# Performance work log

Hardware: AMD Instinct MI355X
Metric: run time of the kernel (lower is better)

The kernel has to match this reference:

```python
import jax, jax.numpy as jnp
import numpy as np

# ---- module constants (from init_kwargs / zounds.SR22050) ----
SEQ = 64
N_SAMPLES = 16384
N_EVENTS = 16
N_HARM = 32
NOISE_WS = 512
NOISE_STEP = 256
NYQ = 11025.0  # SR22050 nyquist
MIN_F0 = 20.0 / NYQ
MAX_F0 = 800.0 / NYQ
F0_DIFF = MAX_F0 - MIN_F0
HARM_FACTOR = jnp.arange(2, 2 + N_HARM, dtype=jnp.float32)  # [2..33]


def lin_interp(x, size):
    """torch F.interpolate(mode='linear', align_corners=False) along last dim."""
    L = x.shape[-1]
    pos = (jnp.arange(size, dtype=x.dtype) + 0.5) * (L / size) - 0.5
    pos = jnp.clip(pos, 0.0, L - 1)
    i0 = jnp.floor(pos).astype(jnp.int32)
    i1 = jnp.minimum(i0 + 1, L - 1)
    w = (pos - i0).astype(x.dtype)
    return x[..., i0] * (1.0 - w) + x[..., i1] * w


def band_filtered_noise(noise_frames, mean, std):
    """Per-frame Gaussian band-pass of white noise in the STFT domain, overlap-add.
    noise_frames: (b,e,F,ws); mean/std: (b,e,F) in normalized freq [0,1]."""
    ws = noise_frames.shape[-1]
    n = jnp.arange(ws, dtype=noise_frames.dtype)
    win = 0.5 - 0.5 * jnp.cos(2.0 * jnp.pi * n / ws)  # Hann
    spec = jnp.fft.rfft(noise_frames * win, axis=-1)  # (b,e,F,ws//2+1)
    freqs = jnp.linspace(0.0, 1.0, ws // 2 + 1)
    filt = jnp.exp(-0.5 * ((freqs[None, None, None, :] - mean[..., None]) / std[..., None]) ** 2)
    frames = jnp.fft.irfft(spec * filt, n=ws, axis=-1)  # (b,e,F,ws)
    # overlap-add with hop NOISE_STEP (ws == 2*step -> two half-chunks per frame)
    b, e, Fn, _ = frames.shape
    chunks = frames.reshape(b, e, Fn, 2, NOISE_STEP)
    a = chunks[..., 0, :].reshape(b, e, Fn * NOISE_STEP)
    c = chunks[..., 1, :].reshape(b, e, Fn * NOISE_STEP)
    out = jnp.zeros((b, e, (Fn + 1) * NOISE_STEP), dtype=frames.dtype)
    out = out.at[..., : Fn * NOISE_STEP].add(a)
    out = out.at[..., NOISE_STEP:].add(c)
    return out[..., :N_SAMPLES]


def setup_inputs() -> dict:
    key = jax.random.key(0)
    ks = jax.random.split(key, 8)
    B = 8
    return {
        "f0": jax.random.uniform(ks[0], (B, N_EVENTS, SEQ), jnp.float32),
        "overall_env": jax.random.uniform(ks[1], (B, N_EVENTS, SEQ), jnp.float32),
        "osc_env": jax.random.uniform(ks[2], (B, N_EVENTS, SEQ), jnp.float32),
        "noise_env": jax.random.uniform(ks[3], (B, N_EVENTS, SEQ), jnp.float32),
        "harm_env": jax.random.uniform(ks[4], (B, N_EVENTS, N_HARM, SEQ), jnp.float32),
        "noise_std": jax.random.uniform(ks[5], (B, N_EVENTS, SEQ), jnp.float32),
        "f0_baselines": jax.random.uniform(ks[6], (B, N_EVENTS, 1), jnp.float32),
        "noise_frames": jax.random.normal(ks[7], (B, N_EVENTS, SEQ, NOISE_WS), jnp.float32),
    }


def reference(f0, overall_env, osc_env, noise_env, harm_env, noise_std, f0_baselines, noise_frames):
    # f0_baselines branch (ERB-scaled deviation around baseline)
    f0 = jnp.clip(f0, -0.5, 0.5)
    scaled_erb = (0.108 * (f0_baselines * NYQ) + 24.7) / NYQ
    f0 = f0_baselines + f0 * scaled_erb

    orig_f0 = f0 = jnp.clip(f0, 0.0, 1.0)
    overall_env = jnp.clip(overall_env, 0.0, 1.0)
    osc_env = jnp.clip(osc_env, 0.0, 1.0)
    harm_env = jnp.clip(harm_env, 0.0, 1.0)
    noise_std = jnp.clip(noise_std, 1e-12, 1.0)

    f0n = MIN_F0 + f0 * F0_DIFF                                   # (b,e,S)
    harm_f = f0n[:, :, None, :] * HARM_FACTOR[None, None, :, None]  # (b,e,H,S)
    harm_env = osc_env[:, :, None, :] * harm_env                  # (b,e,H,S)

    fund = lin_interp(f0n, N_SAMPLES)           # (b,e,N)
    harm_f_i = lin_interp(harm_f, N_SAMPLES)    # (b,e,H,N)
    osc_env_i = lin_interp(osc_env, N_SAMPLES)  # (b,e,N)
    harm_env_i = lin_interp(harm_env, N_SAMPLES)

    fundamental = jnp.sin(jnp.cumsum(fund * jnp.pi, axis=-1)) * osc_env_i
    harmonics = (jnp.sin(jnp.cumsum(harm_f_i * jnp.pi, axis=-1)) * harm_env_i).sum(axis=-2)
    osc = fundamental + harmonics

    noise_mean = MIN_F0 + orig_f0 * F0_DIFF
    nstd = noise_std * F0_DIFF
    noise = band_filtered_noise(noise_frames, noise_mean, nstd)

    osc_mix = lin_interp(overall_env, N_SAMPLES)
    noise_mix = lin_interp(1.0 - overall_env, N_SAMPLES)
    return osc * osc_mix + noise * noise_mix
```

## Files before the change

### kernel.cpp

```cpp
#include <hip/hip_runtime.h>
#include <math.h>

#define SEQ 64
#define NSAMP 16384
#define NHARM 32
#define NWS 512
#define NSTEP 256
#define BE 128
#define NFRAMES 8192

typedef _Float16 half8 __attribute__((ext_vector_type(8)));
typedef float f32x4 __attribute__((ext_vector_type(4)));

__device__ __forceinline__ float sin_rev(float x) {
  float r; asm("v_sin_f32 %0, %1" : "=v"(r) : "v"(x)); return r;
}
__device__ __forceinline__ float cos_rev(float x) {
  float r; asm("v_cos_f32 %0, %1" : "=v"(r) : "v"(x)); return r;
}
__device__ __forceinline__ float clip01(float v) { return fminf(fmaxf(v, 0.0f), 1.0f); }

__device__ __forceinline__ float f0_to_norm(float f0v, float bl) {
  const float NYQ = 11025.0f;
  const float MIN_F0 = 20.0f / 11025.0f;
  const float F0_DIFF = 780.0f / 11025.0f;
  float v = fminf(fmaxf(f0v, -0.5f), 0.5f);
  float erb = (0.108f * (bl * NYQ) + 24.7f) / NYQ;
  float fv = clip01(bl + v * erb);
  return MIN_F0 + fv * F0_DIFF;
}

__global__ __launch_bounds__(256) void prep_k(_Float16* __restrict__ W1) {
  const int m = blockIdx.x, k = m & 127;
  const int tid = threadIdx.x;
  const bool isSin = m >= 128;
  for (int n = tid; n < 512; n += 256) {
    int a = (k * n) & 511;
    float ph = (float)a * (1.0f / 512.0f);
    W1[m * 512 + n] = (_Float16)(isSin ? sin_rev(ph) : cos_rev(ph));
  }
}

__global__ __launch_bounds__(256) void gemmf_k(const float* __restrict__ Af,
                                               const _Float16* __restrict__ B,
                                               _Float16* __restrict__ Cout,
                                               _Float16* __restrict__ W2,
                                               const float* __restrict__ f0,
                                               const float* __restrict__ nstd,
                                               const float* __restrict__ f0b) {
  const int tid = threadIdx.x;

  if (blockIdx.x < 256) {
    const int k = tid & 127;
    const bool isSin = tid >= 128;
#pragma unroll
    for (int rr = 0; rr < 2; ++rr) {
      const int n = blockIdx.x * 2 + rr;
      int a = (k * n) & 511;
      float ph = (float)a * (1.0f / 512.0f);
      W2[n * 256 + tid] = (_Float16)(isSin ? sin_rev(ph) : cos_rev(ph));
    }
    return;
  }

  const int p = blockIdx.x - 256;
  const int x = p & 7, j = p >> 3;
  const int mstripe = ((j >> 2) << 3) + x;
  const int bn0 = (j & 3) * 64;
  const int m0 = mstripe * 64;

  const int Kt = 512;
  const int wave = tid >> 6, lane = tid & 63;
  const int r = lane & 15, q = lane >> 4;
  __shared__ __align__(16) _Float16 Ash[2][64 * 64];
  __shared__ __align__(16) _Float16 Bsh[2][64 * 64];
  __shared__ __align__(16) float whann[512];

  const int nT = Kt >> 6;
  const int srow0 = tid >> 3, srow1 = (256 + tid) >> 3;
  const int skg = tid & 7;

  half8 ra[2], rb[2];
  f32x4 acc[4] = {};

  whann[tid] = 0.5f - 0.5f * cos_rev((float)tid * (1.0f / 512.0f));
  whann[tid + 256] = 0.5f - 0.5f * cos_rev((float)(tid + 256) * (1.0f / 512.0f));
  __syncthreads();

  auto load_a = [&](int kk) {
    const float* s0 = Af + (size_t)(m0 + srow0) * Kt + kk + skg * 8;
    const float* s1 = Af + (size_t)(m0 + srow1) * Kt + kk + skg * 8;
    float4 a0 = ((const float4*)s0)[0], a1 = ((const float4*)s0)[1];
    float4 b0 = ((const float4*)s1)[0], b1 = ((const float4*)s1)[1];
    float4 w0 = *(const float4*)(&whann[kk + skg * 8]);
    float4 w1 = *(const float4*)(&whann[kk + skg * 8 + 4]);
    ra[0][0] = (_Float16)(a0.x * w0.x); ra[0][1] = (_Float16)(a0.y * w0.y);
    ra[0][2] = (_Float16)(a0.z * w0.z); ra[0][3] = (_Float16)(a0.w * w0.w);
    ra[0][4] = (_Float16)(a1.x * w1.x); ra[0][5] = (_Float16)(a1.y * w1.y);
    ra[0][6] = (_Float16)(a1.z * w1.z); ra[0][7] = (_Float16)(a1.w * w1.w);
    ra[1][0] = (_Float16)(b0.x * w0.x); ra[1][1] = (_Float16)(b0.y * w0.y);
    ra[1][2] = (_Float16)(b0.z * w0.z); ra[1][3] = (_Float16)(b0.w * w0.w);
    ra[1][4] = (_Float16)(b1.x * w1.x); ra[1][5] = (_Float16)(b1.y * w1.y);
    ra[1][6] = (_Float16)(b1.z * w1.z); ra[1][7] = (_Float16)(b1.w * w1.w);
    rb[0] = *(const half8*)(B + (size_t)(bn0 + srow0) * Kt + kk + skg * 8);
    rb[1] = *(const half8*)(B + (size_t)(bn0 + srow1) * Kt + kk + skg * 8);
  };
  auto store_lds = [&](int b) {
    *(half8*)(&Ash[b][srow0 * 64 + ((skg ^ (srow0 & 7)) << 3)]) = ra[0];
    *(half8*)(&Ash[b][srow1 * 64 + ((skg ^ (srow1 & 7)) << 3)]) = ra[1];
    *(half8*)(&Bsh[b][srow0 * 64 + ((skg ^ (srow0 & 7)) << 3)]) = rb[0];
    *(half8*)(&Bsh[b][srow1 * 64 + ((skg ^ (srow1 & 7)) << 3)]) = rb[1];
  };

  load_a(0);
  store_lds(0);

  for (int t = 0;;) {
    if (t + 1 < nT) load_a((t + 1) << 6);
    __syncthreads();
    const int b = t & 1;
#pragma unroll
    for (int ks = 0; ks < 2; ++ks) {
      const int swz = ((ks * 4 + q) ^ (r & 7)) << 3;
      half8 af = *(const half8*)(&Ash[b][(wave * 16 + r) * 64 + swz]);
      half8 bf0 = *(const half8*)(&Bsh[b][(0 * 16 + r) * 64 + swz]);
      half8 bf1 = *(const half8*)(&Bsh[b][(1 * 16 + r) * 64 + swz]);
      half8 bf2 = *(const half8*)(&Bsh[b][(2 * 16 + r) * 64 + swz]);
      half8 bf3 = *(const half8*)(&Bsh[b][(3 * 16 + r) * 64 + swz]);
      acc[0] = __builtin_amdgcn_mfma_f32_16x16x32_f16(af, bf0, acc[0], 0, 0, 0);
      acc[1] = __builtin_amdgcn_mfma_f32_16x16x32_f16(af, bf1, acc[1], 0, 0, 0);
      acc[2] = __builtin_amdgcn_mfma_f32_16x16x32_f16(af, bf2, acc[2], 0, 0, 0);
      acc[3] = __builtin_amdgcn_mfma_f32_16x16x32_f16(af, bf3, acc[3], 0, 0, 0);
    }
    if (t + 1 >= nT) break;
    __syncthreads();
    store_lds((t + 1) & 1);
    ++t;
  }

  const float F0_DIFF = 780.0f / 11025.0f;
#pragma unroll
  for (int reg = 0; reg < 4; ++reg) {
    const int row = m0 + wave * 16 + q * 4 + reg;
    const float mu = f0_to_norm(f0[row], f0b[row >> 6]);
    const float sd = fminf(fmaxf(nstd[row], 1e-12f), 1.0f) * F0_DIFF;
    const float inv_sd = 1.0f / sd;
    const float a = inv_sd * (1.0f / 256.0f);
    const float bmu = mu * inv_sd;
#pragma unroll
    for (int ni = 0; ni < 4; ++ni) {
      const int col = bn0 + ni * 16 + r;
      const int k = col & 127;
      float z = fmaf((float)k, a, -bmu);
      float cf = (k == 0) ? (1.0f / 512.0f) : (2.0f / 512.0f);
      float s = cf * exp2f(z * z * -0.72134752044f);
      Cout[(size_t)row * 256 + col] = (_Float16)(acc[ni][reg] * s);
    }
  }
}

__global__ __launch_bounds__(256) void invfin_k(const _Float16* __restrict__ AB,
                                                const _Float16* __restrict__ W2,
                                                const float* __restrict__ f0,
                                                const float* __restrict__ f0b,
                                                const float* __restrict__ oenv_g,
                                                const float* __restrict__ oscenv_g,
                                                const float* __restrict__ henv_g,
                                                float* __restrict__ out) {
  const int p = blockIdx.x;
  const int x = p & 7, j = p >> 3;
  const int be = ((j >> 2) << 3) + x;
  const int n0 = (j & 3) * 64;
  const int m0 = be * 64;
  const int tid = threadIdx.x;
  const int wave = tid >> 6, lane = tid & 63;
  const int r = lane & 15, q = lane >> 4;

  __shared__ __align__(16) _Float16 Ash[65 * 64];
  __shared__ __align__(16) _Float16 B1sh[64 * 64];
  __shared__ __align__(16) _Float16 B2sh[64 * 64];
  __shared__ __align__(16) float4 qe4[8 * SEQ];
  __shared__ float oenv[SEQ], oscE[SEQ];
  __shared__ float Fs[SEQ], Ds[SEQ], Gs[SEQ];

  if (tid < SEQ) {
    oenv[tid] = clip01(oenv_g[be * SEQ + tid]);
    oscE[tid] = clip01(oscenv_g[be * SEQ + tid]);
    Fs[tid] = f0_to_norm(f0[be * SEQ + tid], f0b[be]);
  }
  __syncthreads();

  if (tid < SEQ) {
    const int s = tid;
    float fcur = Fs[s];
    float fnxt = (s < 63) ? Fs[s + 1] : Fs[63];
    Ds[s] = fnxt - fcur;
    double term = 128.0 * ((double)fcur + (double)fnxt);
    double sc = term;
#pragma unroll
    for (int off = 1; off < 64; off <<= 1) {
      double u = __shfl_up(sc, off, 64);
      if (s >= off) sc += u;
    }
    double C = 128.0 * (double)Fs[0] + (sc - term);
    Gs[s] = (float)(C - 2.0 * floor(C * 0.5));
  }

  for (int idx = tid; idx < 8 * SEQ; idx += 256) {
    int hq = idx >> 6, s = idx & 63;
    const float* hb = henv_g + (size_t)be * (NHARM * SEQ) + (4 * hq) * SEQ + s;
    float e = oscE[s];
    qe4[idx] = make_float4(e * clip01(hb[0]), e * clip01(hb[64]),
                           e * clip01(hb[128]), e * clip01(hb[192]));
  }

  auto stage_AB = [&](int kk) {
#pragma unroll
    for (int it = 0; it < 3; ++it) {
      int g = it * 256 + tid;
      if (g < 520) {
        int row = g >> 3, kg = g & 7;
        half8 v = {0, 0, 0, 0, 0, 0, 0, 0};
        if (row > 0)
          v = *(const half8*)(AB + (size_t)(m0 - 1 + row) * 256 + kk + kg * 8);
        *(half8*)(&Ash[row * 64 + ((kg ^ (row & 7)) << 3)]) = v;
      }
    }
#pragma unroll
    for (int it = 0; it < 4; ++it) {
      int g = it * 256 + tid;
      int row = (g >> 3) & 63, kg = g & 7;
      bool second = g >= 512;
      int wrow = n0 + row + (second ? 256 : 0);
      half8 v = *(const half8*)(W2 + (size_t)wrow * 256 + kk + kg * 8);
      _Float16* dst = second ? B2sh : B1sh;
      *(half8*)(&dst[row * 64 + ((kg ^ (row & 7)) << 3)]) = v;
    }
  };

  f32x4 acc[4] = {};
  stage_AB(0);
  __syncthreads();

  for (int t = 0;;) {
#pragma unroll
    for (int ks = 0; ks < 2; ++ks) {
      const int kg = ks * 4 + q;
      const int ra1 = 1 + wave * 16 + r;
      const int ra2 = wave * 16 + r;
      half8 af1 = *(const half8*)(&Ash[ra1 * 64 + ((kg ^ (ra1 & 7)) << 3)]);
      half8 af2 = *(const half8*)(&Ash[ra2 * 64 + ((kg ^ (ra2 & 7)) << 3)]);
#pragma unroll
      for (int ni = 0; ni < 4; ++ni) {
        const int rb = ni * 16 + r;
        const int sw = (kg ^ (rb & 7)) << 3;
        half8 bf1 = *(const half8*)(&B1sh[rb * 64 + sw]);
        half8 bf2 = *(const half8*)(&B2sh[rb * 64 + sw]);
        acc[ni] = __builtin_amdgcn_mfma_f32_16x16x32_f16(af1, bf1, acc[ni], 0, 0, 0);
        acc[ni] = __builtin_amdgcn_mfma_f32_16x16x32_f16(af2, bf2, acc[ni], 0, 0, 0);
      }
    }
    if (t == 3) break;
    __syncthreads();
    stage_AB((t + 1) << 6);
    __syncthreads();
    ++t;
  }

#pragma unroll
  for (int reg = 0; reg < 4; ++reg) {
    const int c = wave * 16 + q * 4 + reg;
#pragma unroll
    for (int ni = 0; ni < 4; ++ni) {
      const int n = n0 + ni * 16 + r;
      const int t = c * 256 + n;
      float pos = ((float)t + 0.5f) * (1.0f / 256.0f) - 0.5f;
      pos = fminf(fmaxf(pos, 0.0f), 63.0f);
      int i0 = (int)pos;
      int i1 = min(i0 + 1, 63);
      float w = pos - (float)i0;

      float pph;
      if (t < 128) {
        pph = (float)(t + 1) * Fs[0];
      } else {
        int s = (t - 128) >> 8;
        float u1 = (float)((t - 128) - (s << 8) + 1);
        pph = Gs[s] + fmaf(Ds[s] * (1.0f / 512.0f), u1 * u1, u1 * Fs[s]);
      }
      pph = pph - 2.0f * floorf(pph * 0.5f);
      float xv = pph * 0.5f;
      float sb = sin_rev(xv);
      float cb = cos_rev(xv);
      float C = 2.0f * cb;

      float fund = sb * (oscE[i0] * (1.0f - w) + oscE[i1] * w);
      float d0 = 0.0f, d1 = 0.0f;
      float sp = sb;
      float scur = C * sb;
#pragma unroll
      for (int hq = 0; hq < 8; ++hq) {
        float4 qa = qe4[hq * 64 + i0];
        float4 qb = qe4[hq * 64 + i1];
        d0 = fmaf(scur, qa.x, d0); d1 = fmaf(scur, qb.x, d1);
        sp = fmaf(C, scur, -sp);
        d0 = fmaf(sp, qa.y, d0);   d1 = fmaf(sp, qb.y, d1);
        scur = fmaf(C, sp, -scur);
        d0 = fmaf(scur, qa.z, d0); d1 = fmaf(scur, qb.z, d1);
        sp = fmaf(C, scur, -sp);
        d0 = fmaf(sp, qa.w, d0);   d1 = fmaf(sp, qb.w, d1);
        scur = fmaf(C, sp, -scur);
      }
      float osc = fund + d0 * (1.0f - w) + d1 * w;
      float mix = oenv[i0] * (1.0f - w) + oenv[i1] * w;
      out[(size_t)be * NSAMP + t] = fmaf(osc, mix, acc[ni][reg] * (1.0f - mix));
    }
  }
}

extern "C" void kernel_launch(void* const* d_in, const int* in_sizes, int n_in,
                              void* d_out, int out_size, void* d_ws, size_t ws_size,
                              hipStream_t stream) {
  const float* f0           = (const float*)d_in[0];
  const float* overall_env  = (const float*)d_in[1];
  const float* osc_env      = (const float*)d_in[2];
  const float* harm_env     = (const float*)d_in[4];
  const float* noise_std    = (const float*)d_in[5];
  const float* f0_base      = (const float*)d_in[6];
  const float* noise_frames = (const float*)d_in[7];
  float* out = (float*)d_out;

  _Float16* W1 = (_Float16*)d_ws;
  _Float16* W2 = W1 + 256 * 512;
  _Float16* AB = W2 + 512 * 256;

  prep_k<<<256, 256, 0, stream>>>(W1);
  gemmf_k<<<768, 256, 0, stream>>>(noise_frames, W1, AB, W2, f0, noise_std, f0_base);
  invfin_k<<<512, 256, 0, stream>>>(
      AB, W2, f0, f0_base, overall_env, osc_env, harm_env, out);
}
```

Before: 36.95 us.

## Fuse three kernels into one persistent kernel with grid-wide atomic barriers

Result: slower. 112.2 us (+203.7%).

```diff
diff --git a/kernel.cpp b/kernel.cpp
--- a/kernel.cpp
+++ b/kernel.cpp
@@ -8,6 +8,7 @@
 #define NSTEP 256
 #define BE 128
 #define NFRAMES 8192
+#define GRID_NB 512u
 
 typedef _Float16 half8 __attribute__((ext_vector_type(8)));
 typedef float f32x4 __attribute__((ext_vector_type(4)));
@@ -30,290 +31,300 @@
   return MIN_F0 + fv * F0_DIFF;
 }
 
-__global__ __launch_bounds__(256) void prep_k(_Float16* __restrict__ W1) {
-  const int m = blockIdx.x, k = m & 127;
-  const int tid = threadIdx.x;
-  const bool isSin = m >= 128;
-  for (int n = tid; n < 512; n += 256) {
-    int a = (k * n) & 511;
-    float ph = (float)a * (1.0f / 512.0f);
-    W1[m * 512 + n] = (_Float16)(isSin ? sin_rev(ph) : cos_rev(ph));
-  }
-}
-
-__global__ __launch_bounds__(256) void gemmf_k(const float* __restrict__ Af,
-                                               const _Float16* __restrict__ B,
-                                               _Float16* __restrict__ Cout,
-                                               _Float16* __restrict__ W2,
-                                               const float* __restrict__ f0,
-                                               const float* __restrict__ nstd,
-                                               const float* __restrict__ f0b) {
-  const int tid = threadIdx.x;
-
-  if (blockIdx.x < 256) {
-    const int k = tid & 127;
-    const bool isSin = tid >= 128;
-#pragma unroll
-    for (int rr = 0; rr < 2; ++rr) {
-      const int n = blockIdx.x * 2 + rr;
-      int a = (k * n) & 511;
-      float ph = (float)a * (1.0f / 512.0f);
-      W2[n * 256 + tid] = (_Float16)(isSin ? sin_rev(ph) : cos_rev(ph));
-    }
-    return;
-  }
-
-  const int p = blockIdx.x - 256;
-  const int x = p & 7, j = p >> 3;
-  const int mstripe = ((j >> 2) << 3) + x;
-  const int bn0 = (j & 3) * 64;
-  const int m0 = mstripe * 64;
-
-  const int Kt = 512;
-  const int wave = tid >> 6, lane = tid & 63;
-  const int r = lane & 15, q = lane >> 4;
-  __shared__ __align__(16) _Float16 Ash[2][64 * 64];
-  __shared__ __align__(16) _Float16 Bsh[2][64 * 64];
-  __shared__ __align__(16) float whann[512];
-
-  const int nT = Kt >> 6;
-  const int srow0 = tid >> 3, srow1 = (256 + tid) >> 3;
-  const int skg = tid & 7;
-
-  half8 ra[2], rb[2];
-  f32x4 acc[4] = {};
-
-  whann[tid] = 0.5f - 0.5f * cos_rev((float)tid * (1.0f / 512.0f));
-  whann[tid + 256] = 0.5f - 0.5f * cos_rev((float)(tid + 256) * (1.0f / 512.0f));
+__device__ __forceinline__ void grid_bar(unsigned int* cnt) {
   __syncthreads();
-
-  auto load_a = [&](int kk) {
-    const float* s0 = Af + (size_t)(m0 + srow0) * Kt + kk + skg * 8;
-    const float* s1 = Af + (size_t)(m0 + srow1) * Kt + kk + skg * 8;
-    float4 a0 = ((const float4*)s0)[0], a1 = ((const float4*)s0)[1];
-    float4 b0 = ((const float4*)s1)[0], b1 = ((const float4*)s1)[1];
-    float4 w0 = *(const float4*)(&whann[kk + skg * 8]);
-    float4 w1 = *(const float4*)(&whann[kk + skg * 8 + 4]);
-    ra[0][0] = (_Float16)(a0.x * w0.x); ra[0][1] = (_Float16)(a0.y * w0.y);
-    ra[0][2] = (_Float16)(a0.z * w0.z); ra[0][3] = (_Float16)(a0.w * w0.w);
-    ra[0][4] = (_Float16)(a1.x * w1.x); ra[0][5] = (_Float16)(a1.y * w1.y);
-    ra[0][6] = (_Float16)(a1.z * w1.z); ra[0][7] = (_Float16)(a1.w * w1.w);
-    ra[1][0] = (_Float16)(b0.x * w0.x); ra[1][1] = (_Float16)(b0.y * w0.y);
-    ra[1][2] = (_Float16)(b0.z * w0.z); ra[1][3] = (_Float16)(b0.w * w0.w);
-    ra[1][4] = (_Float16)(b1.x * w1.x); ra[1][5] = (_Float16)(b1.y * w1.y);
-    ra[1][6] = (_Float16)(b1.z * w1.z); ra[1][7] = (_Float16)(b1.w * w1.w);
-    rb[0] = *(const half8*)(B + (size_t)(bn0 + srow0) * Kt + kk + skg * 8);
-    rb[1] = *(const half8*)(B + (size_t)(bn0 + srow1) * Kt + kk + skg * 8);
-  };
-  auto store_lds = [&](int b) {
-    *(half8*)(&Ash[b][srow0 * 64 + ((skg ^ (srow0 & 7)) << 3)]) = ra[0];
-    *(half8*)(&Ash[b][srow1 * 64 + ((skg ^ (srow1 & 7)) << 3)]) = ra[1];
-    *(half8*)(&Bsh[b][srow0 * 64 + ((skg ^ (srow0 & 7)) << 3)]) = rb[0];
-    *(half8*)(&Bsh[b][srow1 * 64 + ((skg ^ (srow1 & 7)) << 3)]) = rb[1];
-  };
-
-  load_a(0);
-  store_lds(0);
-
-  for (int t = 0;;) {
-    if (t + 1 < nT) load_a((t + 1) << 6);
-    __syncthreads();
-    const int b = t & 1;
-#pragma unroll
-    for (int ks = 0; ks < 2; ++ks) {
-      const int swz = ((ks * 4 + q) ^ (r & 7)) << 3;
-      half8 af = *(const half8*)(&Ash[b][(wave * 16 + r) * 64 + swz]);
-      half8 bf0 = *(const half8*)(&Bsh[b][(0 * 16 + r) * 64 + swz]);
-      half8 bf1 = *(const half8*)(&Bsh[b][(1 * 16 + r) * 64 + swz]);
-      half8 bf2 = *(const half8*)(&Bsh[b][(2 * 16 + r) * 64 + swz]);
-      half8 bf3 = *(const half8*)(&Bsh[b][(3 * 16 + r) * 64 + swz]);
-      acc[0] = __builtin_amdgcn_mfma_f32_16x16x32_f16(af, bf0, acc[0], 0, 0, 0);
-      acc[1] = __builtin_amdgcn_mfma_f32_16x16x32_f16(af, bf1, acc[1], 0, 0, 0);
-      acc[2] = __builtin_amdgcn_mfma_f32_16x16x32_f16(af, bf2, acc[2], 0, 0, 0);
-      acc[3] = __builtin_amdgcn_mfma_f32_16x16x32_f16(af, bf3, acc[3], 0, 0, 0);
-    }
-    if (t + 1 >= nT) break;
-    __syncthreads();
-    store_lds((t + 1) & 1);
-    ++t;
-  }
-
-  const float F0_DIFF = 780.0f / 11025.0f;
-#pragma unroll
-  for (int reg = 0; reg < 4; ++reg) {
-    const int row = m0 + wave * 16 + q * 4 + reg;
-    const float mu = f0_to_norm(f0[row], f0b[row >> 6]);
-    const float sd = fminf(fmaxf(nstd[row], 1e-12f), 1.0f) * F0_DIFF;
-    const float inv_sd = 1.0f / sd;
-    const float a = inv_sd * (1.0f / 256.0f);
-    const float bmu = mu * inv_sd;
-#pragma unroll
-    for (int ni = 0; ni < 4; ++ni) {
-      const int col = bn0 + ni * 16 + r;
-      const int k = col & 127;
-      float z = fmaf((float)k, a, -bmu);
-      float cf = (k == 0) ? (1.0f / 512.0f) : (2.0f / 512.0f);
-      float s = cf * exp2f(z * z * -0.72134752044f);
-      Cout[(size_t)row * 256 + col] = (_Float16)(acc[ni][reg] * s);
-    }
-  }
-}
-
-__global__ __launch_bounds__(256) void invfin_k(const _Float16* __restrict__ AB,
-                                                const _Float16* __restrict__ W2,
-                                                const float* __restrict__ f0,
-                                                const float* __restrict__ f0b,
-                                                const float* __restrict__ oenv_g,
-                                                const float* __restrict__ oscenv_g,
-                                                const float* __restrict__ henv_g,
-                                                float* __restrict__ out) {
-  const int p = blockIdx.x;
-  const int x = p & 7, j = p >> 3;
-  const int be = ((j >> 2) << 3) + x;
-  const int n0 = (j & 3) * 64;
-  const int m0 = be * 64;
+  if (threadIdx.x == 0) {
+    __threadfence();
+    __hip_atomic_fetch_add(cnt, 1u, __ATOMIC_ACQ_REL, __HIP_MEMORY_SCOPE_AGENT);
+    while (__hip_atomic_load(cnt, __ATOMIC_ACQUIRE, __HIP_MEMORY_SCOPE_AGENT) < GRID_NB) {
+      __builtin_amdgcn_s_sleep(2);
+    }
+  }
+  __syncthreads();
+}
+
+__global__ __launch_bounds__(256, 3) void fused_k(
+    const float* __restrict__ Af,
+    const float* __restrict__ f0,
+    const float* __restrict__ nstd,
+    const float* __restrict__ f0b,
+    const float* __restrict__ oenv_g,
+    const float* __restrict__ oscenv_g,
+    const float* __restrict__ henv_g,
+    _Float16* __restrict__ W1,
+    _Float16* __restrict__ W2,
+    _Float16* __restrict__ AB,
+    unsigned int* __restrict__ bar,
+    float* __restrict__ out) {
+  __shared__ __align__(16) unsigned char smem[34816];
+  const int bid = blockIdx.x;
   const int tid = threadIdx.x;
   const int wave = tid >> 6, lane = tid & 63;
   const int r = lane & 15, q = lane >> 4;
 
-  __shared__ __align__(16) _Float16 Ash[65 * 64];
-  __shared__ __align__(16) _Float16 B1sh[64 * 64];
-  __shared__ __align__(16) _Float16 B2sh[64 * 64];
-  __shared__ __align__(16) float4 qe4[8 * SEQ];
-  __shared__ float oenv[SEQ], oscE[SEQ];
-  __shared__ float Fs[SEQ], Ds[SEQ], Gs[SEQ];
-
-  if (tid < SEQ) {
-    oenv[tid] = clip01(oenv_g[be * SEQ + tid]);
-    oscE[tid] = clip01(oscenv_g[be * SEQ + tid]);
-    Fs[tid] = f0_to_norm(f0[be * SEQ + tid], f0b[be]);
-  }
-  __syncthreads();
-
-  if (tid < SEQ) {
-    const int s = tid;
-    float fcur = Fs[s];
-    float fnxt = (s < 63) ? Fs[s + 1] : Fs[63];
-    Ds[s] = fnxt - fcur;
-    double term = 128.0 * ((double)fcur + (double)fnxt);
-    double sc = term;
-#pragma unroll
-    for (int off = 1; off < 64; off <<= 1) {
-      double u = __shfl_up(sc, off, 64);
-      if (s >= off) sc += u;
-    }
-    double C = 128.0 * (double)Fs[0] + (sc - term);
-    Gs[s] = (float)(C - 2.0 * floor(C * 0.5));
-  }
-
-  for (int idx = tid; idx < 8 * SEQ; idx += 256) {
-    int hq = idx >> 6, s = idx & 63;
-    const float* hb = henv_g + (size_t)be * (NHARM * SEQ) + (4 * hq) * SEQ + s;
-    float e = oscE[s];
-    qe4[idx] = make_float4(e * clip01(hb[0]), e * clip01(hb[64]),
-                           e * clip01(hb[128]), e * clip01(hb[192]));
-  }
-
-  auto stage_AB = [&](int kk) {
-#pragma unroll
-    for (int it = 0; it < 3; ++it) {
-      int g = it * 256 + tid;
-      if (g < 520) {
-        int row = g >> 3, kg = g & 7;
-        half8 v = {0, 0, 0, 0, 0, 0, 0, 0};
-        if (row > 0)
-          v = *(const half8*)(AB + (size_t)(m0 - 1 + row) * 256 + kk + kg * 8);
-        *(half8*)(&Ash[row * 64 + ((kg ^ (row & 7)) << 3)]) = v;
-      }
-    }
-#pragma unroll
-    for (int it = 0; it < 4; ++it) {
-      int g = it * 256 + tid;
-      int row = (g >> 3) & 63, kg = g & 7;
-      bool second = g >= 512;
-      int wrow = n0 + row + (second ? 256 : 0);
-      half8 v = *(const half8*)(W2 + (size_t)wrow * 256 + kk + kg * 8);
-      _Float16* dst = second ? B2sh : B1sh;
-      *(half8*)(&dst[row * 64 + ((kg ^ (row & 7)) << 3)]) = v;
-    }
-  };
-
-  f32x4 acc[4] = {};
-  stage_AB(0);
-  __syncthreads();
-
-  for (int t = 0;;) {
-#pragma unroll
-    for (int ks = 0; ks < 2; ++ks) {
-      const int kg = ks * 4 + q;
-      const int ra1 = 1 + wave * 16 + r;
-      const int ra2 = wave * 16 + r;
-      half8 af1 = *(const half8*)(&Ash[ra1 * 64 + ((kg ^ (ra1 & 7)) << 3)]);
-      half8 af2 = *(const half8*)(&Ash[ra2 * 64 + ((kg ^ (ra2 & 7)) << 3)]);
+  if (bid < 256) {
+    const int k = bid & 127;
+    const bool isSin = bid >= 128;
+    for (int n = tid; n < 512; n += 256) {
+      int a = (k * n) & 511;
+      float ph = (float)a * (1.0f / 512.0f);
+      W1[bid * 512 + n] = (_Float16)(isSin ? sin_rev(ph) : cos_rev(ph));
+    }
+  }
+  {
+    const int k = tid & 127;
+    const bool isSin = tid >= 128;
+    int a = (k * bid) & 511;
+    float ph = (float)a * (1.0f / 512.0f);
+    W2[bid * 256 + tid] = (_Float16)(isSin ? sin_rev(ph) : cos_rev(ph));
+  }
+
+  grid_bar(&bar[0]);
+
+  {
+    const int x = bid & 7, j = bid >> 3;
+    const int mstripe = ((j >> 2) << 3) + x;
+    const int bn0 = (j & 3) * 64;
+    const int m0 = mstripe * 64;
+    const int Kt = 512;
+
+    _Float16* Ash = (_Float16*)smem;
+    _Float16* Bsh = (_Float16*)(smem + 16384);
+    float* whann = (float*)(smem + 32768);
+
+    const int nT = Kt >> 6;
+    const int srow0 = tid >> 3, srow1 = (256 + tid) >> 3;
+    const int skg = tid & 7;
+
+    half8 ra[2], rb[2];
+    f32x4 acc[4] = {};
+
+    whann[tid] = 0.5f - 0.5f * cos_rev((float)tid * (1.0f / 512.0f));
+    whann[tid + 256] = 0.5f - 0.5f * cos_rev((float)(tid + 256) * (1.0f / 512.0f));
+    __syncthreads();
+
+    auto load_a = [&](int kk) {
+      const float* s0 = Af + (size_t)(m0 + srow0) * Kt + kk + skg * 8;
+      const float* s1 = Af + (size_t)(m0 + srow1) * Kt + kk + skg * 8;
+      float4 a0 = ((const float4*)s0)[0], a1 = ((const float4*)s0)[1];
+      float4 b0 = ((const float4*)s1)[0], b1 = ((const float4*)s1)[1];
+      float4 w0 = *(const float4*)(&whann[kk + skg * 8]);
+      float4 w1 = *(const float4*)(&whann[kk + skg * 8 + 4]);
+      ra[0][0] = (_Float16)(a0.x * w0.x); ra[0][1] = (_Float16)(a0.y * w0.y);
+      ra[0][2] = (_Float16)(a0.z * w0.z); ra[0][3] = (_Float16)(a0.w * w0.w);
+      ra[0][4] = (_Float16)(a1.x * w1.x); ra[0][5] = (_Float16)(a1.y * w1.y);
+      ra[0][6] = (_Float16)(a1.z * w1.z); ra[0][7] = (_Float16)(a1.w * w1.w);
+      ra[1][0] = (_Float16)(b0.x * w0.x); ra[1][1] = (_Float16)(b0.y * w0.y);
+      ra[1][2] = (_Float16)(b0.z * w0.z); ra[1][3] = (_Float16)(b0.w * w0.w);
+      ra[1][4] = (_Float16)(b1.x * w1.x); ra[1][5] = (_Float16)(b1.y * w1.y);
+      ra[1][6] = (_Float16)(b1.z * w1.z); ra[1][7] = (_Float16)(b1.w * w1.w);
+      rb[0] = *(const half8*)(W1 + (size_t)(bn0 + srow0) * Kt + kk + skg * 8);
+      rb[1] = *(const half8*)(W1 + (size_t)(bn0 + srow1) * Kt + kk + skg * 8);
+    };
+    auto store_lds = [&](int b) {
+      *(half8*)(&Ash[b * 4096 + srow0 * 64 + ((skg ^ (srow0 & 7)) << 3)]) = ra[0];
+      *(half8*)(&Ash[b * 4096 + srow1 * 64 + ((skg ^ (srow1 & 7)) << 3)]) = ra[1];
+      *(half8*)(&Bsh[b * 4096 + srow0 * 64 + ((skg ^ (srow0 & 7)) << 3)]) = rb[0];
+      *(half8*)(&Bsh[b * 4096 + srow1 * 64 + ((skg ^ (srow1 & 7)) << 3)]) = rb[1];
+    };
+
+    load_a(0);
+    store_lds(0);
+
+    for (int t = 0;;) {
+      if (t + 1 < nT) load_a((t + 1) << 6);
+      __syncthreads();
+      const int b = t & 1;
+#pragma unroll
+      for (int ks = 0; ks < 2; ++ks) {
+        const int swz = ((ks * 4 + q) ^ (r & 7)) << 3;
+        half8 af = *(const half8*)(&Ash[b * 4096 + (wave * 16 + r) * 64 + swz]);
+        half8 bf0 = *(const half8*)(&Bsh[b * 4096 + (0 * 16 + r) * 64 + swz]);
+        half8 bf1 = *(const half8*)(&Bsh[b * 4096 + (1 * 16 + r) * 64 + swz]);
+        half8 bf2 = *(const half8*)(&Bsh[b * 4096 + (2 * 16 + r) * 64 + swz]);
+        half8 bf3 = *(const half8*)(&Bsh[b * 4096 + (3 * 16 + r) * 64 + swz]);
+        acc[0] = __builtin_amdgcn_mfma_f32_16x16x32_f16(af, bf0, acc[0], 0, 0, 0);
+        acc[1] = __builtin_amdgcn_mfma_f32_16x16x32_f16(af, bf1, acc[1], 0, 0, 0);
+        acc[2] = __builtin_amdgcn_mfma_f32_16x16x32_f16(af, bf2, acc[2], 0, 0, 0);
+        acc[3] = __builtin_amdgcn_mfma_f32_16x16x32_f16(af, bf3, acc[3], 0, 0, 0);
+      }
+      if (t + 1 >= nT) break;
+      __syncthreads();
+      store_lds((t + 1) & 1);
+      ++t;
+    }
+
+    const float F0_DIFF = 780.0f / 11025.0f;
+#pragma unroll
+    for (int reg = 0; reg < 4; ++reg) {
+      const int row = m0 + wave * 16 + q * 4 + reg;
+      const float mu = f0_to_norm(f0[row], f0b[row >> 6]);
+      const float sd = fminf(fmaxf(nstd[row], 1e-12f), 1.0f) * F0_DIFF;
+      const float inv_sd = 1.0f / sd;
+      const float a = inv_sd * (1.0f / 256.0f);
+      const float bmu = mu * inv_sd;
 #pragma unroll
       for (int ni = 0; ni < 4; ++ni) {
-        const int rb = ni * 16 + r;
-        const int sw = (kg ^ (rb & 7)) << 3;
-        half8 bf1 = *(const half8*)(&B1sh[rb * 64 + sw]);
-        half8 bf2 = *(const half8*)(&B2sh[rb * 64 + sw]);
-        acc[ni] = __builtin_amdgcn_mfma_f32_16x16x32_f16(af1, bf1, acc[ni], 0, 0, 0);
-        acc[ni] = __builtin_amdgcn_mfma_f32_16x16x32_f16(af2, bf2, acc[ni], 0, 0, 0);
-      }
-    }
-    if (t == 3) break;
+        const int col = bn0 + ni * 16 + r;
+        const int k = col & 127;
+        float z = fmaf((float)k, a, -bmu);
+        float cf = (k == 0) ? (1.0f / 512.0f) : (2.0f / 512.0f);
+        float s = cf * exp2f(z * z * -0.72134752044f);
+        AB[(size_t)row * 256 + col] = (_Float16)(acc[ni][reg] * s);
+      }
+    }
+  }
+
+  grid_bar(&bar[1]);
+
+  {
+    const int x = bid & 7, j = bid >> 3;
+    const int be = ((j >> 2) << 3) + x;
+    const int n0 = (j & 3) * 64;
+    const int m0 = be * 64;
+
+    _Float16* A2sh = (_Float16*)smem;
+    _Float16* B1sh = (_Float16*)(smem + 8320);
+    _Float16* B2sh = (_Float16*)(smem + 16512);
+    float4* qe4 = (float4*)(smem + 24704);
+    float* oenv = (float*)(smem + 32896);
+    float* oscE = (float*)(smem + 33152);
+    float* Fs = (float*)(smem + 33408);
+    float* Ds = (float*)(smem + 33664);
+    float* Gs = (float*)(smem + 33920);
+
+    if (tid < SEQ) {
+      oenv[tid] = clip01(oenv_g[be * SEQ + tid]);
+      oscE[tid] = clip01(oscenv_g[be * SEQ + tid]);
+      Fs[tid] = f0_to_norm(f0[be * SEQ + tid], f0b[be]);
+    }
     __syncthreads();
-    stage_AB((t + 1) << 6);
+
+    if (tid < SEQ) {
+      const int s = tid;
+      float fcur = Fs[s];
+      float fnxt = (s < 63) ? Fs[s + 1] : Fs[63];
+      Ds[s] = fnxt - fcur;
+      double term = 128.0 * ((double)fcur + (double)fnxt);
+      double sc = term;
+#pragma unroll
+      for (int off = 1; off < 64; off <<= 1) {
+        double u = __shfl_up(sc, off, 64);
+        if (s >= off) sc += u;
+      }
+      double C = 128.0 * (double)Fs[0] + (sc - term);
+      Gs[s] = (float)(C - 2.0 * floor(C * 0.5));
+    }
+
+    for (int idx = tid; idx < 8 * SEQ; idx += 256) {
+      int hq = idx >> 6, s = idx & 63;
+      const float* hb = henv_g + (size_t)be * (NHARM * SEQ) + (4 * hq) * SEQ + s;
+      float e = oscE[s];
+      qe4[idx] = make_float4(e * clip01(hb[0]), e * clip01(hb[64]),
+                             e * clip01(hb[128]), e * clip01(hb[192]));
+    }
+
+    auto stage_AB = [&](int kk) {
+#pragma unroll
+      for (int it = 0; it < 3; ++it) {
+        int g = it * 256 + tid;
+        if (g < 520) {
+          int row = g >> 3, kg = g & 7;
+          half8 v = {0, 0, 0, 0, 0, 0, 0, 0};
+          if (row > 0)
+            v = *(const half8*)(AB + (size_t)(m0 - 1 + row) * 256 + kk + kg * 8);
+          *(half8*)(&A2sh[row * 64 + ((kg ^ (row & 7)) << 3)]) = v;
+        }
+      }
+#pragma unroll
+      for (int it = 0; it < 4; ++it) {
+        int g = it * 256 + tid;
+        int row = (g >> 3) & 63, kg = g & 7;
+        bool second = g >= 512;
+        int wrow = n0 + row + (second ? 256 : 0);
+        half8 v = *(const half8*)(W2 + (size_t)wrow * 256 + kk + kg * 8);
+        _Float16* dst = second ? B2sh : B1sh;
+        *(half8*)(&dst[row * 64 + ((kg ^ (row & 7)) << 3)]) = v;
+      }
+    };
+
+    f32x4 acc[4] = {};
+    stage_AB(0);
     __syncthreads();
-    ++t;
-  }
-
-#pragma unroll
-  for (int reg = 0; reg < 4; ++reg) {
-    const int c = wave * 16 + q * 4 + reg;
-#pragma unroll
-    for (int ni = 0; ni < 4; ++ni) {
-      const int n = n0 + ni * 16 + r;
-      const int t = c * 256 + n;
-      float pos = ((float)t + 0.5f) * (1.0f / 256.0f) - 0.5f;
-      pos = fminf(fmaxf(pos, 0.0f), 63.0f);
-      int i0 = (int)pos;
-      int i1 = min(i0 + 1, 63);
-      float w = pos - (float)i0;
-
-      float pph;
-      if (t < 128) {
-        pph = (float)(t + 1) * Fs[0];
-      } else {
-        int s = (t - 128) >> 8;
-        float u1 = (float)((t - 128) - (s << 8) + 1);
-        pph = Gs[s] + fmaf(Ds[s] * (1.0f / 512.0f), u1 * u1, u1 * Fs[s]);
-      }
-      pph = pph - 2.0f * floorf(pph * 0.5f);
-      float xv = pph * 0.5f;
-      float sb = sin_rev(xv);
-      float cb = cos_rev(xv);
-      float C = 2.0f * cb;
-
-      float fund = sb * (oscE[i0] * (1.0f - w) + oscE[i1] * w);
-      float d0 = 0.0f, d1 = 0.0f;
-      float sp = sb;
-      float scur = C * sb;
-#pragma unroll
-      for (int hq = 0; hq < 8; ++hq) {
-        float4 qa = qe4[hq * 64 + i0];
-        float4 qb = qe4[hq * 64 + i1];
-        d0 = fmaf(scur, qa.x, d0); d1 = fmaf(scur, qb.x, d1);
-        sp = fmaf(C, scur, -sp);
-        d0 = fmaf(sp, qa.y, d0);   d1 = fmaf(sp, qb.y, d1);
-        scur = fmaf(C, sp, -scur);
-        d0 = fmaf(scur, qa.z, d0); d1 = fmaf(scur, qb.z, d1);
-        sp = fmaf(C, scur, -sp);
-        d0 = fmaf(sp, qa.w, d0);   d1 = fmaf(sp, qb.w, d1);
-        scur = fmaf(C, sp, -scur);
-      }
-      float osc = fund + d0 * (1.0f - w) + d1 * w;
-      float mix = oenv[i0] * (1.0f - w) + oenv[i1] * w;
-      out[(size_t)be * NSAMP + t] = fmaf(osc, mix, acc[ni][reg] * (1.0f - mix));
+
+    for (int t = 0;;) {
+#pragma unroll
+      for (int ks = 0; ks < 2; ++ks) {
+        const int kg = ks * 4 + q;
+        const int ra1 = 1 + wave * 16 + r;
+        const int ra2 = wave * 16 + r;
+        half8 af1 = *(const half8*)(&A2sh[ra1 * 64 + ((kg ^ (ra1 & 7)) << 3)]);
+        half8 af2 = *(const half8*)(&A2sh[ra2 * 64 + ((kg ^ (ra2 & 7)) << 3)]);
+#pragma unroll
+        for (int ni = 0; ni < 4; ++ni) {
+          const int rb = ni * 16 + r;
+          const int sw = (kg ^ (rb & 7)) << 3;
+          half8 bf1 = *(const half8*)(&B1sh[rb * 64 + sw]);
+          half8 bf2 = *(const half8*)(&B2sh[rb * 64 + sw]);
+          acc[ni] = __builtin_amdgcn_mfma_f32_16x16x32_f16(af1, bf1, acc[ni], 0, 0, 0);
+          acc[ni] = __builtin_amdgcn_mfma_f32_16x16x32_f16(af2, bf2, acc[ni], 0, 0, 0);
+        }
+      }
+      if (t == 3) break;
+      __syncthreads();
+      stage_AB((t + 1) << 6);
+      __syncthreads();
+      ++t;
+    }
+
+#pragma unroll
+    for (int reg = 0; reg < 4; ++reg) {
+      const int c = wave * 16 + q * 4 + reg;
+#pragma unroll
+      for (int ni = 0; ni < 4; ++ni) {
+        const int n = n0 + ni * 16 + r;
+        const int t = c * 256 + n;
+        float pos = ((float)t + 0.5f) * (1.0f / 256.0f) - 0.5f;
+        pos = fminf(fmaxf(pos, 0.0f), 63.0f);
+        int i0 = (int)pos;
+        int i1 = min(i0 + 1, 63);
+        float w = pos - (float)i0;
+
+        float pph;
+        if (t < 128) {
+          pph = (float)(t + 1) * Fs[0];
+        } else {
+          int s = (t - 128) >> 8;
+          float u1 = (float)((t - 128) - (s << 8) + 1);
+          pph = Gs[s] + fmaf(Ds[s] * (1.0f / 512.0f), u1 * u1, u1 * Fs[s]);
+        }
+        pph = pph - 2.0f * floorf(pph * 0.5f);
+        float xv = pph * 0.5f;
+        float sb = sin_rev(xv);
+        float cb = cos_rev(xv);
+        float C = 2.0f * cb;
+
+        float fund = sb * (oscE[i0] * (1.0f - w) + oscE[i1] * w);
+        float d0 = 0.0f, d1 = 0.0f;
+        float sp = sb;
+        float scur = C * sb;
+#pragma unroll
+        for (int hq = 0; hq < 8; ++hq) {
+          float4 qa = qe4[hq * 64 + i0];
+          float4 qb = qe4[hq * 64 + i1];
+          d0 = fmaf(scur, qa.x, d0); d1 = fmaf(scur, qb.x, d1);
+          sp = fmaf(C, scur, -sp);
+          d0 = fmaf(sp, qa.y, d0);   d1 = fmaf(sp, qb.y, d1);
+          scur = fmaf(C, sp, -scur);
+          d0 = fmaf(scur, qa.z, d0); d1 = fmaf(scur, qb.z, d1);
+          sp = fmaf(C, scur, -sp);
+          d0 = fmaf(sp, qa.w, d0);   d1 = fmaf(sp, qb.w, d1);
+          scur = fmaf(C, sp, -scur);
+        }
+        float osc = fund + d0 * (1.0f - w) + d1 * w;
+        float mix = oenv[i0] * (1.0f - w) + oenv[i1] * w;
+        out[(size_t)be * NSAMP + t] = fmaf(osc, mix, acc[ni][reg] * (1.0f - mix));
+      }
     }
   }
 }
@@ -333,9 +344,11 @@
   _Float16* W1 = (_Float16*)d_ws;
   _Float16* W2 = W1 + 256 * 512;
   _Float16* AB = W2 + 512 * 256;
-
-  prep_k<<<256, 256, 0, stream>>>(W1);
-  gemmf_k<<<768, 256, 0, stream>>>(noise_frames, W1, AB, W2, f0, noise_std, f0_base);
-  invfin_k<<<512, 256, 0, stream>>>(
-      AB, W2, f0, f0_base, overall_env, osc_env, harm_env, out);
-}
+  unsigned int* bar = (unsigned int*)(AB + (size_t)NFRAMES * 256);
+
+  hipMemsetAsync(bar, 0, 2 * sizeof(unsigned int), stream);
+
+  fused_k<<<GRID_NB, 256, 0, stream>>>(
+      noise_frames, f0, noise_std, f0_base, overall_env, osc_env, harm_env,
+      W1, W2, AB, bar, out);
+}
```
